# Optimization experiments

Measured on AMD Instinct MI355X. Metric: run time of the kernel, lower is better.

## Reference

```python
import jax, jax.numpy as jnp
import numpy as np

D_MODEL = 2048
N_HEADS = 32
N_KV_HEADS = 8
HEAD_DIM = D_MODEL // N_HEADS
ROPE_BASE = 10000.0

def setup_inputs() -> dict:
    key = jax.random.key(0)
    ks = jax.random.split(key, 5)
    B, S = 1, 2048
    x = jax.random.normal(ks[0], (B, S, D_MODEL), dtype=jnp.float32)
    sc = 1.0 / np.sqrt(D_MODEL)
    Wq = jax.random.normal(ks[1], (D_MODEL, D_MODEL), dtype=jnp.float32) * sc
    Wk = jax.random.normal(ks[2], (N_KV_HEADS * HEAD_DIM, D_MODEL), dtype=jnp.float32) * sc
    Wv = jax.random.normal(ks[3], (N_KV_HEADS * HEAD_DIM, D_MODEL), dtype=jnp.float32) * sc
    Wo = jax.random.normal(ks[4], (D_MODEL, D_MODEL), dtype=jnp.float32) * sc
    return {"x": x, "Wq": Wq, "Wk": Wk, "Wv": Wv, "Wo": Wo}

def _rope_cos_sin(seq_len, dtype):
    inv_freq = 1.0 / (ROPE_BASE ** (jnp.arange(0, HEAD_DIM, 2, dtype=jnp.float32) / HEAD_DIM))
    t = jnp.arange(seq_len, dtype=jnp.float32)
    freqs = jnp.einsum('i,j->ij', t, inv_freq)          # [S, hd/2]
    emb = jnp.concatenate([freqs, freqs], axis=-1)      # [S, hd]
    return jnp.cos(emb).astype(dtype), jnp.sin(emb).astype(dtype)

def _rotate_half(x):
    x1, x2 = x[..., : HEAD_DIM // 2], x[..., HEAD_DIM // 2 :]
    return jnp.concatenate([-x2, x1], axis=-1)

def reference(x, Wq, Wk, Wv, Wo):
    B, S, _ = x.shape
    scale = HEAD_DIM ** -0.5
    # projections (Linear: x @ W.T)
    q = (x @ Wq.T).reshape(B, S, N_HEADS, HEAD_DIM).transpose(0, 2, 1, 3)      # [B,H,S,hd]
    k = (x @ Wk.T).reshape(B, S, N_KV_HEADS, HEAD_DIM).transpose(0, 2, 1, 3)   # [B,Hkv,S,hd]
    v = (x @ Wv.T).reshape(B, S, N_KV_HEADS, HEAD_DIM).transpose(0, 2, 1, 3)
    cos, sin = _rope_cos_sin(S, x.dtype)                # [S,hd], broadcasts over B,H
    q = q * cos + _rotate_half(q) * sin
    k = k * cos + _rotate_half(k) * sin
    rep = N_HEADS // N_KV_HEADS
    k = jnp.repeat(k, rep, axis=1)                       # [B,H,S,hd]
    v = jnp.repeat(v, rep, axis=1)
    scores = jnp.einsum('bhqd,bhkd->bhqk', q, k) * scale # [B,H,S,S]
    attn = jax.nn.softmax(scores, axis=-1)
    out = jnp.einsum('bhqk,bhkd->bhqd', attn, v)         # [B,H,S,hd]
    out = out.transpose(0, 2, 1, 3).reshape(B, S, D_MODEL)
    return out @ Wo.T
```

## Files before the change

kernel.cpp:

```cpp
#include <hip/hip_runtime.h>
#include <hip/hip_bf16.h>
#include <cmath>

typedef __bf16 bf16_t;
typedef __attribute__((ext_vector_type(8))) __bf16 bf16x8;
typedef __attribute__((ext_vector_type(4))) float f32x4;
typedef __attribute__((ext_vector_type(4))) short s16x4;

#define S_LEN 2048
#define DMODEL 2048
#define KVDIM 512
#define NHEADS 32
#define NKV 8
#define HDIM 64

__device__ inline f32x4 zero4() { f32x4 z; z[0]=0.f; z[1]=0.f; z[2]=0.f; z[3]=0.f; return z; }

__global__ void convert_all(const float* __restrict__ s0, bf16_t* __restrict__ d0,
                            const float* __restrict__ s1, bf16_t* __restrict__ d1,
                            const float* __restrict__ s2, bf16_t* __restrict__ d2,
                            const float* __restrict__ s3, bf16_t* __restrict__ d3,
                            const float* __restrict__ s4, bf16_t* __restrict__ d4) {
  int b = blockIdx.x;
  const float* src; bf16_t* dst; int boff;
  if      (b < 2048) { src = s0; dst = d0; boff = b; }
  else if (b < 4096) { src = s1; dst = d1; boff = b - 2048; }
  else if (b < 4608) { src = s2; dst = d2; boff = b - 4096; }
  else if (b < 5120) { src = s3; dst = d3; boff = b - 4608; }
  else               { src = s4; dst = d4; boff = b - 5120; }
  int idx = (boff * 256 + threadIdx.x) * 8;
  bf16x8 v;
#pragma unroll
  for (int j = 0; j < 8; j++) v[j] = (bf16_t)src[idx + j];
  *(bf16x8*)(dst + idx) = v;
}

template <int BN, bool F32OUT>
__device__ __forceinline__ void gemm_core(const bf16_t* __restrict__ A,
                                          const bf16_t* __restrict__ Bt,
                                          void* __restrict__ Cout,
                                          int N, int K, int bm, int bn) {
  constexpr int NT_W = BN / 32;
  __shared__ __attribute__((aligned(16))) bf16_t As[128 * 64];
  __shared__ __attribute__((aligned(16))) bf16_t Bs[BN * 64];
  const int tid  = threadIdx.x;
  const int wave = tid >> 6, lane = tid & 63;
  const int wm = wave >> 1, wn = wave & 1;
  const int quad = lane >> 4, lr = lane & 15;
  const int srow = lane >> 3, scol = lane & 7;

  f32x4 acc[4][NT_W];
#pragma unroll
  for (int i = 0; i < 4; i++)
#pragma unroll
    for (int j = 0; j < NT_W; j++) acc[i][j] = zero4();

  for (int k0 = 0; k0 < K; k0 += 64) {
#pragma unroll
    for (int i = 0; i < 4; i++) {
      const bf16_t* gA = A + (size_t)(bm + i * 32 + wave * 8 + srow) * K + k0 + scol * 8;
      bf16_t* lA = As + (i * 32 + wave * 8) * 64;
      __builtin_amdgcn_global_load_lds((const __attribute__((address_space(1))) void*)gA,
                                       (__attribute__((address_space(3))) void*)lA, 16, 0, 0);
    }
#pragma unroll
    for (int i = 0; i < BN / 32; i++) {
      const bf16_t* gB = Bt + (size_t)(bn + i * 32 + wave * 8 + srow) * K + k0 + scol * 8;
      bf16_t* lB = Bs + (i * 32 + wave * 8) * 64;
      __builtin_amdgcn_global_load_lds((const __attribute__((address_space(1))) void*)gB,
                                       (__attribute__((address_space(3))) void*)lB, 16, 0, 0);
    }
    __syncthreads();
#pragma unroll
    for (int ks = 0; ks < 2; ks++) {
      bf16x8 a[4], b[NT_W];
#pragma unroll
      for (int mt = 0; mt < 4; mt++)
        a[mt] = *(const bf16x8*)&As[(wm * 64 + mt * 16 + lr) * 64 + ks * 32 + quad * 8];
#pragma unroll
      for (int nt = 0; nt < NT_W; nt++)
        b[nt] = *(const bf16x8*)&Bs[(wn * (BN / 2) + nt * 16 + lr) * 64 + ks * 32 + quad * 8];
#pragma unroll
      for (int mt = 0; mt < 4; mt++)
#pragma unroll
        for (int nt = 0; nt < NT_W; nt++)
          acc[mt][nt] = __builtin_amdgcn_mfma_f32_16x16x32_bf16(a[mt], b[nt], acc[mt][nt], 0, 0, 0);
    }
    __syncthreads();
  }

#pragma unroll
  for (int mt = 0; mt < 4; mt++)
#pragma unroll
    for (int nt = 0; nt < NT_W; nt++)
#pragma unroll
      for (int r = 0; r < 4; r++) {
        int row = bm + wm * 64 + mt * 16 + quad * 4 + r;
        int col = bn + wn * (BN / 2) + nt * 16 + lr;
        if (F32OUT) ((float*)Cout)[(size_t)row * N + col] = acc[mt][nt][r];
        else ((bf16_t*)Cout)[(size_t)row * N + col] = (bf16_t)acc[mt][nt][r];
      }
}

__global__ __launch_bounds__(256) void gemm_proj(const bf16_t* __restrict__ xb,
                                                 const bf16_t* __restrict__ Wqb,
                                                 const bf16_t* __restrict__ Wkb,
                                                 const bf16_t* __restrict__ Wvb,
                                                 bf16_t* __restrict__ qb,
                                                 bf16_t* __restrict__ kb,
                                                 bf16_t* __restrict__ vb) {
  int b = blockIdx.x;
  if (b < 512) {
    gemm_core<64, false>(xb, Wqb, qb, 2048, 2048, (b >> 5) * 128, (b & 31) * 64);
  } else if (b < 640) {
    int r = b - 512;
    gemm_core<64, false>(xb, Wkb, kb, 512, 2048, (r >> 3) * 128, (r & 7) * 64);
  } else {
    int r = b - 640;
    gemm_core<64, false>(Wvb, xb, vb, 2048, 2048, (r >> 5) * 128, (r & 31) * 64);
  }
}

__global__ __launch_bounds__(256) void gemm_out(const bf16_t* __restrict__ A,
                                                const bf16_t* __restrict__ Bt,
                                                float* __restrict__ C) {
  int b = blockIdx.x;
  gemm_core<64, true>(A, Bt, C, 2048, 2048, (b >> 5) * 128, (b & 31) * 64);
}

__global__ void rope_k(bf16_t* __restrict__ kb) {
  int idx = blockIdx.x * 256 + threadIdx.x;
  int s = idx >> 8;
  int rem = idx & 255;
  int head = rem >> 5;
  int i = rem & 31;
  float freq = __expf(-0.2878231366f * (float)i);
  float ang = (float)s * freq;
  float sn, cs;
  sincosf(ang, &sn, &cs);
  size_t base = (size_t)s * KVDIM + head * 64 + i;
  float x0 = (float)kb[base];
  float x1 = (float)kb[base + 32];
  kb[base]      = (bf16_t)(x0 * cs - x1 * sn);
  kb[base + 32] = (bf16_t)(x1 * cs + x0 * sn);
}

__global__ __launch_bounds__(256) void attn_kernel(const bf16_t* __restrict__ q,
                                                   const bf16_t* __restrict__ k,
                                                   const bf16_t* __restrict__ vT,
                                                   bf16_t* __restrict__ out) {
  __shared__ __attribute__((aligned(16))) bf16_t Ks[2][128 * 64];
  __shared__ __attribute__((aligned(16))) bf16_t Vs[2][64 * 128];
  const int tid  = threadIdx.x;
  const int wave = tid >> 6, lane = tid & 63;
  const int quad = lane >> 4, lr = lane & 15;
  const int srow = lane >> 3, scol = lane & 7;
  const int vrow = lane >> 4, vcol = lane & 15;
  const int cg = scol ^ srow;
  const int qt = blockIdx.x, h = blockIdx.y;
  const int hkv = h >> 2;
  const int qrow0 = qt * 128 + wave * 32;
  const int sw = lr & 7;
  const int c0 = (quad ^ sw) * 8;
  const int c1 = ((quad + 4) ^ sw) * 8;

  bf16x8 aqA0, aqA1, aqB0, aqB1;
#pragma unroll
  for (int set = 0; set < 2; set++) {
    int row = qrow0 + set * 16 + lr;
    const bf16_t* qp = q + (size_t)row * DMODEL + h * HDIM + quad * 8;
    bf16x8 r0 = *(const bf16x8*)qp;
    bf16x8 r1 = *(const bf16x8*)(qp + 32);
    float srow_f = (float)row;
    bf16x8 a0, a1;
#pragma unroll
    for (int j = 0; j < 8; j++) {
      float freq = __expf(-0.2878231366f * (float)(quad * 8 + j));
      float sn, cs;
      sincosf(srow_f * freq, &sn, &cs);
      float x0 = (float)r0[j], x1 = (float)r1[j];
      a0[j] = (bf16_t)(x0 * cs - x1 * sn);
      a1[j] = (bf16_t)(x1 * cs + x0 * sn);
    }
    if (set == 0) { aqA0 = a0; aqA1 = a1; } else { aqB0 = a0; aqB1 = a1; }
  }

  f32x4 OA[4], OB[4];
  float lA = 0.f, lB = 0.f;
#pragma unroll
  for (int mt = 0; mt < 4; mt++) { OA[mt] = zero4(); OB[mt] = zero4(); }

#define STAGE_TILE(BUF, KT)                                                              \
  {                                                                                      \
    _Pragma("unroll")                                                                    \
    for (int j = 0; j < 4; j++) {                                                        \
      const bf16_t* gK = k + (size_t)((KT) + wave * 32 + j * 8 + srow) * KVDIM +         \
                         hkv * HDIM + cg * 8;                                            \
      bf16_t* lK = Ks[BUF] + (wave * 32 + j * 8) * 64;                                   \
      __builtin_amdgcn_global_load_lds((const __attribute__((address_space(1))) void*)gK,\
                                       (__attribute__((address_space(3))) void*)lK, 16, 0, 0); \
    }                                                                                    \
    _Pragma("unroll")                                                                    \
    for (int j = 0; j < 4; j++) {                                                        \
      int dg = wave * 16 + j * 4 + vrow;                                                 \
      int cgv = vcol ^ (dg & 7);                                                         \
      const bf16_t* gV = vT + (size_t)(hkv * HDIM + dg) * S_LEN + (KT) + cgv * 8;        \
      bf16_t* lV = Vs[BUF] + (wave * 16 + j * 4) * 128;                                  \
      __builtin_amdgcn_global_load_lds((const __attribute__((address_space(1))) void*)gV,\
                                       (__attribute__((address_space(3))) void*)lV, 16, 0, 0); \
    }                                                                                    \
  }

  STAGE_TILE(0, 0);
  __syncthreads();

  int cur = 0;
  for (int kt = 0; kt < S_LEN; kt += 128) {
    if (kt + 128 < S_LEN) STAGE_TILE(cur ^ 1, kt + 128);
    const bf16_t* Kc = Ks[cur];
    const bf16_t* Vc = Vs[cur];

    s16x4 bpA[8], bpB[8];
#pragma unroll
    for (int nt = 0; nt < 8; nt++) {
      const int rk = (nt * 16 + lr) * 64;
      bf16x8 kb0 = *(const bf16x8*)&Kc[rk + c0];
      bf16x8 kb1 = *(const bf16x8*)&Kc[rk + c1];
      f32x4 sA = zero4(), sB = zero4();
      __builtin_amdgcn_s_setprio(1);
      sA = __builtin_amdgcn_mfma_f32_16x16x32_bf16(kb0, aqA0, sA, 0, 0, 0);
      sA = __builtin_amdgcn_mfma_f32_16x16x32_bf16(kb1, aqA1, sA, 0, 0, 0);
      sB = __builtin_amdgcn_mfma_f32_16x16x32_bf16(kb0, aqB0, sB, 0, 0, 0);
      sB = __builtin_amdgcn_mfma_f32_16x16x32_bf16(kb1, aqB1, sB, 0, 0, 0);
      __builtin_amdgcn_s_setprio(0);
#pragma unroll
      for (int r = 0; r < 4; r++) {
        float pA = __builtin_amdgcn_exp2f(sA[r] * 0.1803368801f);
        lA += pA;
        bpA[nt][r] = __builtin_bit_cast(short, (bf16_t)pA);
        float pB = __builtin_amdgcn_exp2f(sB[r] * 0.1803368801f);
        lB += pB;
        bpB[nt][r] = __builtin_bit_cast(short, (bf16_t)pB);
      }
    }
#pragma unroll
    for (int nt = 0; nt < 8; nt++) {
      const int slot = ((nt * 2 + (quad >> 1)) ^ sw) * 8 + (quad & 1) * 4;
      s16x4 av[4];
#pragma unroll
      for (int mt = 0; mt < 4; mt++)
        av[mt] = *(const s16x4*)&Vc[(mt * 16 + lr) * 128 + slot];
      __builtin_amdgcn_s_setprio(1);
#pragma unroll
      for (int mt = 0; mt < 4; mt++) {
        OA[mt] = __builtin_amdgcn_mfma_f32_16x16x16bf16_1k(av[mt], bpA[nt], OA[mt], 0, 0, 0);
        OB[mt] = __builtin_amdgcn_mfma_f32_16x16x16bf16_1k(av[mt], bpB[nt], OB[mt], 0, 0, 0);
      }
      __builtin_amdgcn_s_setprio(0);
    }
    __syncthreads();
    cur ^= 1;
  }
#undef STAGE_TILE

  lA += __shfl_xor(lA, 16);
  lA += __shfl_xor(lA, 32);
  lB += __shfl_xor(lB, 16);
  lB += __shfl_xor(lB, 32);
  float invA = 1.f / lA;
  float invB = 1.f / lB;

#pragma unroll
  for (int mt = 0; mt < 4; mt++) {
    s16x4 ovA, ovB;
#pragma unroll
    for (int r = 0; r < 4; r++) {
      ovA[r] = __builtin_bit_cast(short, (bf16_t)(OA[mt][r] * invA));
      ovB[r] = __builtin_bit_cast(short, (bf16_t)(OB[mt][r] * invB));
    }
    *(s16x4*)&out[(size_t)(qrow0 + lr) * DMODEL + h * HDIM + mt * 16 + quad * 4] = ovA;
    *(s16x4*)&out[(size_t)(qrow0 + 16 + lr) * DMODEL + h * HDIM + mt * 16 + quad * 4] = ovB;
  }
}

extern "C" void kernel_launch(void* const* d_in, const int* in_sizes, int n_in,
                              void* d_out, int out_size, void* d_ws, size_t ws_size,
                              hipStream_t stream) {
  (void)in_sizes; (void)n_in; (void)out_size; (void)ws_size;
  const float* x  = (const float*)d_in[0];
  const float* Wq = (const float*)d_in[1];
  const float* Wk = (const float*)d_in[2];
  const float* Wv = (const float*)d_in[3];
  const float* Wo = (const float*)d_in[4];

  bf16_t* xb  = (bf16_t*)d_ws;
  bf16_t* Wqb = xb  + (size_t)4 * 1024 * 1024;
  bf16_t* Wkb = Wqb + (size_t)4 * 1024 * 1024;
  bf16_t* Wvb = Wkb + (size_t)1024 * 1024;
  bf16_t* qb  = Wvb + (size_t)1024 * 1024;
  bf16_t* kb  = qb  + (size_t)4 * 1024 * 1024;
  bf16_t* vb  = kb  + (size_t)1024 * 1024;
  bf16_t* Wob = vb  + (size_t)1024 * 1024;
  bf16_t* ab  = xb;

  dim3 blk(256);
  convert_all<<<7168, blk, 0, stream>>>(x, xb, Wq, Wqb, Wk, Wkb, Wv, Wvb, Wo, Wob);
  gemm_proj<<<768, blk, 0, stream>>>(xb, Wqb, Wkb, Wvb, qb, kb, vb);
  rope_k<<<2048, blk, 0, stream>>>(kb);
  attn_kernel<<<dim3(S_LEN / 128, NHEADS), blk, 0, stream>>>(qb, kb, vb, ab);
  gemm_out<<<512, blk, 0, stream>>>(ab, Wob, (float*)d_out);
}
```

Baseline: 236.6 us.

## Split-K the projection and output GEMMs with fp32 partials and combine kernels

```diff
diff --git a/kernel.cpp b/kernel.cpp
--- a/kernel.cpp
+++ b/kernel.cpp
@@ -39,7 +39,8 @@
 __device__ __forceinline__ void gemm_core(const bf16_t* __restrict__ A,
                                           const bf16_t* __restrict__ Bt,
                                           void* __restrict__ Cout,
-                                          int N, int K, int bm, int bn) {
+                                          int N, int K, int kbeg, int kend,
+                                          int bm, int bn) {
   constexpr int NT_W = BN / 32;
   __shared__ __attribute__((aligned(16))) bf16_t As[128 * 64];
   __shared__ __attribute__((aligned(16))) bf16_t Bs[BN * 64];
@@ -55,7 +56,7 @@
 #pragma unroll
     for (int j = 0; j < NT_W; j++) acc[i][j] = zero4();
 
-  for (int k0 = 0; k0 < K; k0 += 64) {
+  for (int k0 = kbeg; k0 < kend; k0 += 64) {
 #pragma unroll
     for (int i = 0; i < 4; i++) {
       const bf16_t* gA = A + (size_t)(bm + i * 32 + wave * 8 + srow) * K + k0 + scol * 8;
@@ -111,13 +112,13 @@
                                                  bf16_t* __restrict__ vb) {
   int b = blockIdx.x;
   if (b < 512) {
-    gemm_core<64, false>(xb, Wqb, qb, 2048, 2048, (b >> 5) * 128, (b & 31) * 64);
+    gemm_core<64, false>(xb, Wqb, qb, 2048, 2048, 0, 2048, (b >> 5) * 128, (b & 31) * 64);
   } else if (b < 640) {
     int r = b - 512;
-    gemm_core<64, false>(xb, Wkb, kb, 512, 2048, (r >> 3) * 128, (r & 7) * 64);
+    gemm_core<64, false>(xb, Wkb, kb, 512, 2048, 0, 2048, (r >> 3) * 128, (r & 7) * 64);
   } else {
     int r = b - 640;
-    gemm_core<64, false>(Wvb, xb, vb, 2048, 2048, (r >> 5) * 128, (r & 31) * 64);
+    gemm_core<64, false>(Wvb, xb, vb, 2048, 2048, 0, 2048, (r >> 5) * 128, (r & 31) * 64);
   }
 }
 
@@ -125,7 +126,7 @@
                                                 const bf16_t* __restrict__ Bt,
                                                 float* __restrict__ C) {
   int b = blockIdx.x;
-  gemm_core<64, true>(A, Bt, C, 2048, 2048, (b >> 5) * 128, (b & 31) * 64);
+  gemm_core<64, true>(A, Bt, C, 2048, 2048, 0, 2048, (b >> 5) * 128, (b & 31) * 64);
 }
 
 __global__ void rope_k(bf16_t* __restrict__ kb) {
@@ -143,6 +144,107 @@
   float x1 = (float)kb[base + 32];
   kb[base]      = (bf16_t)(x0 * cs - x1 * sn);
   kb[base + 32] = (bf16_t)(x1 * cs + x0 * sn);
+}
+
+__global__ __launch_bounds__(256) void gemm_proj_sk(const bf16_t* __restrict__ xb,
+                                                    const bf16_t* __restrict__ Wqb,
+                                                    const bf16_t* __restrict__ Wkb,
+                                                    const bf16_t* __restrict__ Wvb,
+                                                    float* __restrict__ Pq0, float* __restrict__ Pq1,
+                                                    float* __restrict__ Pk0, float* __restrict__ Pk1,
+                                                    float* __restrict__ Pv0, float* __restrict__ Pv1) {
+  int b = blockIdx.x;
+  int half = b >= 768;
+  int r = b - 768 * half;
+  int kb_ = half * 1024, ke = kb_ + 1024;
+  if (r < 512) {
+    gemm_core<64, true>(xb, Wqb, half ? Pq1 : Pq0, 2048, 2048, kb_, ke,
+                        (r >> 5) * 128, (r & 31) * 64);
+  } else if (r < 640) {
+    int r2 = r - 512;
+    gemm_core<64, true>(xb, Wkb, half ? Pk1 : Pk0, 512, 2048, kb_, ke,
+                        (r2 >> 3) * 128, (r2 & 7) * 64);
+  } else {
+    int r3 = r - 640;
+    gemm_core<64, true>(Wvb, xb, half ? Pv1 : Pv0, 2048, 2048, kb_, ke,
+                        (r3 >> 5) * 128, (r3 & 31) * 64);
+  }
+}
+
+__global__ void proj_combine(const float* __restrict__ Pq0, const float* __restrict__ Pq1,
+                             const float* __restrict__ Pk0, const float* __restrict__ Pk1,
+                             const float* __restrict__ Pv0, const float* __restrict__ Pv1,
+                             bf16_t* __restrict__ qb, bf16_t* __restrict__ kb,
+                             bf16_t* __restrict__ vb) {
+  int b = blockIdx.x, tid = threadIdx.x;
+  if (b < 2048) {
+    int idx = (b * 256 + tid) * 8;
+    f32x4 a0 = *(const f32x4*)&Pq0[idx], a1 = *(const f32x4*)&Pq0[idx + 4];
+    f32x4 c0 = *(const f32x4*)&Pq1[idx], c1 = *(const f32x4*)&Pq1[idx + 4];
+    bf16x8 o;
+#pragma unroll
+    for (int r = 0; r < 4; r++) {
+      o[r]     = (bf16_t)(a0[r] + c0[r]);
+      o[4 + r] = (bf16_t)(a1[r] + c1[r]);
+    }
+    *(bf16x8*)&qb[idx] = o;
+  } else if (b < 2560) {
+    int idx = ((b - 2048) * 256 + tid) * 8;
+    f32x4 a0 = *(const f32x4*)&Pv0[idx], a1 = *(const f32x4*)&Pv0[idx + 4];
+    f32x4 c0 = *(const f32x4*)&Pv1[idx], c1 = *(const f32x4*)&Pv1[idx + 4];
+    bf16x8 o;
+#pragma unroll
+    for (int r = 0; r < 4; r++) {
+      o[r]     = (bf16_t)(a0[r] + c0[r]);
+      o[4 + r] = (bf16_t)(a1[r] + c1[r]);
+    }
+    *(bf16x8*)&vb[idx] = o;
+  } else {
+    int p = (b - 2560) * 256 + tid;
+    int s = p >> 5, rem = p & 31;
+    int head = rem >> 2, c = rem & 3;
+    int i0 = c * 8;
+    int base = s * KVDIM + head * 64 + i0;
+    f32x4 xa0 = *(const f32x4*)&Pk0[base],      xa1 = *(const f32x4*)&Pk0[base + 4];
+    f32x4 xb0 = *(const f32x4*)&Pk1[base],      xb1 = *(const f32x4*)&Pk1[base + 4];
+    f32x4 ya0 = *(const f32x4*)&Pk0[base + 32], ya1 = *(const f32x4*)&Pk0[base + 36];
+    f32x4 yb0 = *(const f32x4*)&Pk1[base + 32], yb1 = *(const f32x4*)&Pk1[base + 36];
+    float sf = (float)s;
+    bf16x8 lo, hi;
+#pragma unroll
+    for (int j = 0; j < 8; j++) {
+      float x0 = (j < 4 ? xa0[j] + xb0[j] : xa1[j - 4] + xb1[j - 4]);
+      float x1 = (j < 4 ? ya0[j] + yb0[j] : ya1[j - 4] + yb1[j - 4]);
+      float freq = __expf(-0.2878231366f * (float)(i0 + j));
+      float sn, cs;
+      sincosf(sf * freq, &sn, &cs);
+      lo[j] = (bf16_t)(x0 * cs - x1 * sn);
+      hi[j] = (bf16_t)(x1 * cs + x0 * sn);
+    }
+    *(bf16x8*)&kb[base] = lo;
+    *(bf16x8*)&kb[base + 32] = hi;
+  }
+}
+
+__global__ __launch_bounds__(256) void gemm_out_sk(const bf16_t* __restrict__ A,
+                                                   const bf16_t* __restrict__ Bt,
+                                                   float* __restrict__ P0,
+                                                   float* __restrict__ P1) {
+  int b = blockIdx.x;
+  int half = b >= 512;
+  int r = b - 512 * half;
+  gemm_core<64, true>(A, Bt, half ? P1 : P0, 2048, 2048, half * 1024, half * 1024 + 1024,
+                      (r >> 5) * 128, (r & 31) * 64);
+}
+
+__global__ void out_combine(float* __restrict__ dOut, const float* __restrict__ P1) {
+  int idx = (blockIdx.x * 256 + threadIdx.x) * 8;
+  f32x4 a0 = *(const f32x4*)&dOut[idx], a1 = *(const f32x4*)&dOut[idx + 4];
+  f32x4 b0 = *(const f32x4*)&P1[idx],   b1 = *(const f32x4*)&P1[idx + 4];
+#pragma unroll
+  for (int r = 0; r < 4; r++) { a0[r] += b0[r]; a1[r] += b1[r]; }
+  *(f32x4*)&dOut[idx] = a0;
+  *(f32x4*)&dOut[idx + 4] = a1;
 }
 
 __global__ __launch_bounds__(256) void attn_kernel(const bf16_t* __restrict__ q,
@@ -286,7 +388,7 @@
 extern "C" void kernel_launch(void* const* d_in, const int* in_sizes, int n_in,
                               void* d_out, int out_size, void* d_ws, size_t ws_size,
                               hipStream_t stream) {
-  (void)in_sizes; (void)n_in; (void)out_size; (void)ws_size;
+  (void)in_sizes; (void)n_in; (void)out_size;
   const float* x  = (const float*)d_in[0];
   const float* Wq = (const float*)d_in[1];
   const float* Wk = (const float*)d_in[2];
@@ -305,8 +407,26 @@
 
   dim3 blk(256);
   convert_all<<<7168, blk, 0, stream>>>(x, xb, Wq, Wqb, Wk, Wkb, Wv, Wvb, Wo, Wob);
-  gemm_proj<<<768, blk, 0, stream>>>(xb, Wqb, Wkb, Wvb, qb, kb, vb);
-  rope_k<<<2048, blk, 0, stream>>>(kb);
-  attn_kernel<<<dim3(S_LEN / 128, NHEADS), blk, 0, stream>>>(qb, kb, vb, ab);
-  gemm_out<<<512, blk, 0, stream>>>(ab, Wob, (float*)d_out);
-}
+
+  const size_t MB = 1024 * 1024;
+  if (ws_size >= 88 * MB) {
+    float* Pq0 = (float*)((char*)d_ws + 40 * MB);
+    float* Pq1 = Pq0 + (size_t)4 * 1024 * 1024;
+    float* Pk0 = Pq1 + (size_t)4 * 1024 * 1024;
+    float* Pk1 = Pk0 + (size_t)1024 * 1024;
+    float* Pv0 = Pk1 + (size_t)1024 * 1024;
+    float* Pv1 = Pv0 + (size_t)1024 * 1024;
+    float* Po1 = Pq0;
+
+    gemm_proj_sk<<<1536, blk, 0, stream>>>(xb, Wqb, Wkb, Wvb, Pq0, Pq1, Pk0, Pk1, Pv0, Pv1);
+    proj_combine<<<2816, blk, 0, stream>>>(Pq0, Pq1, Pk0, Pk1, Pv0, Pv1, qb, kb, vb);
+    attn_kernel<<<dim3(S_LEN / 128, NHEADS), blk, 0, stream>>>(qb, kb, vb, ab);
+    gemm_out_sk<<<1024, blk, 0, stream>>>(ab, Wob, (float*)d_out, Po1);
+    out_combine<<<2048, blk, 0, stream>>>((float*)d_out, Po1);
+  } else {
+    gemm_proj<<<768, blk, 0, stream>>>(xb, Wqb, Wkb, Wvb, qb, kb, vb);
+    rope_k<<<2048, blk, 0, stream>>>(kb);
+    attn_kernel<<<dim3(S_LEN / 128, NHEADS), blk, 0, stream>>>(qb, kb, vb, ab);
+    gemm_out<<<512, blk, 0, stream>>>(ab, Wob, (float*)d_out);
+  }
+}
```

After: 248.6 us. 1.05x slower.

## Double-buffer GEMM LDS tiles and remap blocks to XCD-local tiles

Applied to the files above, without the earlier changes.

```diff
diff --git a/kernel.cpp b/kernel.cpp
--- a/kernel.cpp
+++ b/kernel.cpp
@@ -41,8 +41,8 @@
                                           void* __restrict__ Cout,
                                           int N, int K, int bm, int bn) {
   constexpr int NT_W = BN / 32;
-  __shared__ __attribute__((aligned(16))) bf16_t As[128 * 64];
-  __shared__ __attribute__((aligned(16))) bf16_t Bs[BN * 64];
+  __shared__ __attribute__((aligned(16))) bf16_t As[2][128 * 64];
+  __shared__ __attribute__((aligned(16))) bf16_t Bs[2][BN * 64];
   const int tid  = threadIdx.x;
   const int wave = tid >> 6, lane = tid & 63;
   const int wm = wave >> 1, wn = wave & 1;
@@ -55,31 +55,39 @@
 #pragma unroll
     for (int j = 0; j < NT_W; j++) acc[i][j] = zero4();
 
+#define G_STAGE(BUF, K0)                                                                 \
+  {                                                                                      \
+    _Pragma("unroll")                                                                    \
+    for (int i = 0; i < 4; i++) {                                                        \
+      const bf16_t* gA = A + (size_t)(bm + i * 32 + wave * 8 + srow) * K + (K0) + scol * 8; \
+      bf16_t* lA = As[BUF] + (i * 32 + wave * 8) * 64;                                   \
+      __builtin_amdgcn_global_load_lds((const __attribute__((address_space(1))) void*)gA,\
+                                       (__attribute__((address_space(3))) void*)lA, 16, 0, 0); \
+    }                                                                                    \
+    _Pragma("unroll")                                                                    \
+    for (int i = 0; i < BN / 32; i++) {                                                  \
+      const bf16_t* gB = Bt + (size_t)(bn + i * 32 + wave * 8 + srow) * K + (K0) + scol * 8; \
+      bf16_t* lB = Bs[BUF] + (i * 32 + wave * 8) * 64;                                   \
+      __builtin_amdgcn_global_load_lds((const __attribute__((address_space(1))) void*)gB,\
+                                       (__attribute__((address_space(3))) void*)lB, 16, 0, 0); \
+    }                                                                                    \
+  }
+
+  G_STAGE(0, 0);
+  __syncthreads();
+
+  int cur = 0;
   for (int k0 = 0; k0 < K; k0 += 64) {
-#pragma unroll
-    for (int i = 0; i < 4; i++) {
-      const bf16_t* gA = A + (size_t)(bm + i * 32 + wave * 8 + srow) * K + k0 + scol * 8;
-      bf16_t* lA = As + (i * 32 + wave * 8) * 64;
-      __builtin_amdgcn_global_load_lds((const __attribute__((address_space(1))) void*)gA,
-                                       (__attribute__((address_space(3))) void*)lA, 16, 0, 0);
-    }
-#pragma unroll
-    for (int i = 0; i < BN / 32; i++) {
-      const bf16_t* gB = Bt + (size_t)(bn + i * 32 + wave * 8 + srow) * K + k0 + scol * 8;
-      bf16_t* lB = Bs + (i * 32 + wave * 8) * 64;
-      __builtin_amdgcn_global_load_lds((const __attribute__((address_space(1))) void*)gB,
-                                       (__attribute__((address_space(3))) void*)lB, 16, 0, 0);
-    }
-    __syncthreads();
+    if (k0 + 64 < K) G_STAGE(cur ^ 1, k0 + 64);
 #pragma unroll
     for (int ks = 0; ks < 2; ks++) {
       bf16x8 a[4], b[NT_W];
 #pragma unroll
       for (int mt = 0; mt < 4; mt++)
-        a[mt] = *(const bf16x8*)&As[(wm * 64 + mt * 16 + lr) * 64 + ks * 32 + quad * 8];
+        a[mt] = *(const bf16x8*)&As[cur][(wm * 64 + mt * 16 + lr) * 64 + ks * 32 + quad * 8];
 #pragma unroll
       for (int nt = 0; nt < NT_W; nt++)
-        b[nt] = *(const bf16x8*)&Bs[(wn * (BN / 2) + nt * 16 + lr) * 64 + ks * 32 + quad * 8];
+        b[nt] = *(const bf16x8*)&Bs[cur][(wn * (BN / 2) + nt * 16 + lr) * 64 + ks * 32 + quad * 8];
 #pragma unroll
       for (int mt = 0; mt < 4; mt++)
 #pragma unroll
@@ -87,7 +95,9 @@
           acc[mt][nt] = __builtin_amdgcn_mfma_f32_16x16x32_bf16(a[mt], b[nt], acc[mt][nt], 0, 0, 0);
     }
     __syncthreads();
-  }
+    cur ^= 1;
+  }
+#undef G_STAGE
 
 #pragma unroll
   for (int mt = 0; mt < 4; mt++)
@@ -100,6 +110,12 @@
         if (F32OUT) ((float*)Cout)[(size_t)row * N + col] = acc[mt][nt][r];
         else ((bf16_t*)Cout)[(size_t)row * N + col] = (bf16_t)acc[mt][nt][r];
       }
+}
+
+__device__ __forceinline__ void xcd_tile(int b, int& bm, int& bn) {
+  int c = b & 7, t = b >> 3;
+  bm = (((c >> 2) << 3) + (t >> 3)) * 128;
+  bn = (((c & 3) << 3) + (t & 7)) * 64;
 }
 
 __global__ __launch_bounds__(256) void gemm_proj(const bf16_t* __restrict__ xb,
@@ -111,7 +127,9 @@
                                                  bf16_t* __restrict__ vb) {
   int b = blockIdx.x;
   if (b < 512) {
-    gemm_core<64, false>(xb, Wqb, qb, 2048, 2048, (b >> 5) * 128, (b & 31) * 64);
+    int bm, bn;
+    xcd_tile(b, bm, bn);
+    gemm_core<64, false>(xb, Wqb, qb, 2048, 2048, bm, bn);
   } else if (b < 640) {
     int r = b - 512;
     gemm_core<64, false>(xb, Wkb, kb, 512, 2048, (r >> 3) * 128, (r & 7) * 64);
@@ -124,8 +142,9 @@
 __global__ __launch_bounds__(256) void gemm_out(const bf16_t* __restrict__ A,
                                                 const bf16_t* __restrict__ Bt,
                                                 float* __restrict__ C) {
-  int b = blockIdx.x;
-  gemm_core<64, true>(A, Bt, C, 2048, 2048, (b >> 5) * 128, (b & 31) * 64);
+  int bm, bn;
+  xcd_tile(blockIdx.x, bm, bn);
+  gemm_core<64, true>(A, Bt, C, 2048, 2048, bm, bn);
 }
 
 __global__ void rope_k(bf16_t* __restrict__ kb) {
```

After: 236.7 us. Within noise of the previous version (+0.0%).
